# Kernel optimization log

Measured on AMD Instinct MI355X. Metric: run time of the kernel, lower is better.

The kernel has to match this reference:

```python
import jax, jax.numpy as jnp
import numpy as np

N_NODES = 100000
N_EDGES = 1600000
NIN = 128
NOUT = 128


def setup_inputs() -> dict:
    key = jax.random.key(0)
    k1, k2, k3, k4, k5 = jax.random.split(key, 5)
    x = jax.random.normal(k1, (N_NODES, NIN), dtype=jnp.float32)
    edge_index = jax.random.randint(k2, (2, N_EDGES), 0, N_NODES, dtype=jnp.int32)
    edge_attr = jax.random.uniform(k3, (N_EDGES,), dtype=jnp.float32)
    # GCNConv linear weight (glorot-ish scale) and bias
    W = jax.random.normal(k4, (NIN, NOUT), dtype=jnp.float32) / np.sqrt(NIN)
    b = jnp.zeros((NOUT,), dtype=jnp.float32)
    return {"x": x, "edge_index": edge_index, "edge_attr": edge_attr, "W": W, "b": b}


def reference(x, edge_index, edge_attr, W, b):
    # PyG GCNConv: out = D^{-1/2} (A + I) D^{-1/2} X W + b
    # edge_attr is accepted by the wrapper's forward but ignored.
    N = x.shape[0]
    src, dst = edge_index[0], edge_index[1]
    # add self-loops
    loops = jnp.arange(N, dtype=edge_index.dtype)
    src = jnp.concatenate([src, loops])
    dst = jnp.concatenate([dst, loops])
    # degree over destination nodes (unit edge weights + self loops)
    deg = jax.ops.segment_sum(jnp.ones_like(dst, dtype=x.dtype), dst, num_segments=N)
    dinv = jnp.where(deg > 0, jax.lax.rsqrt(deg), 0.0)
    norm = dinv[src] * dinv[dst]  # [E + N]
    h = x @ W  # [N, NOUT] — project before aggregation (PyG order)
    msgs = h[src] * norm[:, None]  # [E + N, NOUT] gathered messages
    out = jax.ops.segment_sum(msgs, dst, num_segments=N) + b
    return out
```

## Files before the change

kernel.cpp:

```cpp
#include <hip/hip_runtime.h>
#include <hip/hip_bf16.h>


#define NIN 128
#define NOUT 128
#define NPART 8
#define SCAT_B 256
#define MAXD 64

typedef __attribute__((ext_vector_type(8))) short short8;
typedef __attribute__((ext_vector_type(4))) float f32x4;

__device__ __forceinline__ float bf2f(unsigned short u) {
    unsigned v = ((unsigned)u) << 16;
    return __uint_as_float(v);
}
__device__ __forceinline__ unsigned short f2bf(float f) {
    unsigned u = __float_as_uint(f);
    unsigned r = 0x7FFFu + ((u >> 16) & 1u);
    return (unsigned short)((u + r) >> 16);
}

__global__ void k_scatter(const int* __restrict__ ei, int* __restrict__ cnt,
                          int* __restrict__ adj, int E, int N) {
    int p = blockIdx.x & (NPART - 1);
    int c = blockIdx.x / NPART;
    int PS = (N + NPART - 1) / NPART;
    int lo = p * PS, hi = min(N, lo + PS);
    int chunkE = (E + SCAT_B - 1) / SCAT_B;
    int e0 = c * chunkE, e1 = min(E, e0 + chunkE);
    for (int e = e0 + threadIdx.x; e < e1; e += 256) {
        int d = ei[E + e];
        if (d >= lo && d < hi) {
            int s = ei[e];
            int pos = atomicAdd(&cnt[d], 1);
            if (pos < MAXD) adj[(size_t)d * MAXD + pos] = s;
        }
    }
}

#define WT_PITCH 136
__global__ __launch_bounds__(256) void k_gemm(const float* __restrict__ x,
                                              const float* __restrict__ W,
                                              const int* __restrict__ cnt,
                                              unsigned short* __restrict__ h, int N) {
    __shared__ unsigned short Wt[128 * WT_PITCH];
    for (int idx = threadIdx.x; idx < NIN * NOUT; idx += 256) {
        int k = idx >> 7, n = idx & 127;
        Wt[n * WT_PITCH + k] = f2bf(W[idx]);
    }
    __syncthreads();

    int wave = threadIdx.x >> 6, lane = threadIdx.x & 63;
    int node_base = blockIdx.x * 64 + wave * 16;
    if (node_base >= N) return;

    int c = lane & 15, quad = lane >> 4;

    short8 a[4];
    const float4* xrow = (const float4*)(x + (size_t)(node_base + c) * NIN + quad * 8);
    #pragma unroll
    for (int kt = 0; kt < 4; kt++) {
        float4 f0 = xrow[kt * 8];
        float4 f1 = xrow[kt * 8 + 1];
        short8 af;
        af[0] = (short)f2bf(f0.x); af[1] = (short)f2bf(f0.y);
        af[2] = (short)f2bf(f0.z); af[3] = (short)f2bf(f0.w);
        af[4] = (short)f2bf(f1.x); af[5] = (short)f2bf(f1.y);
        af[6] = (short)f2bf(f1.z); af[7] = (short)f2bf(f1.w);
        a[kt] = af;
    }

    f32x4 acc[8];
    #pragma unroll
    for (int nt = 0; nt < 8; nt++) acc[nt] = (f32x4)(0.0f);

    #pragma unroll
    for (int nt = 0; nt < 8; nt++) {
        const unsigned short* wp = &Wt[(nt * 16 + c) * WT_PITCH + quad * 8];
        #pragma unroll
        for (int kt = 0; kt < 4; kt++) {
            short8 bfrag = *(const short8*)(wp + kt * 32);
            acc[nt] = __builtin_amdgcn_mfma_f32_16x16x32_bf16(a[kt], bfrag, acc[nt], 0, 0, 0);
        }
    }

    float dv[4];
    #pragma unroll
    for (int r = 0; r < 4; r++)
        dv[r] = rsqrtf((float)(cnt[node_base + quad * 4 + r] + 1));

    #pragma unroll
    for (int nt = 0; nt < 8; nt++) {
        #pragma unroll
        for (int r = 0; r < 4; r++) {
            int node = node_base + quad * 4 + r;
            h[(size_t)node * NOUT + nt * 16 + c] = f2bf(acc[nt][r] * dv[r]);
        }
    }
}

__global__ __launch_bounds__(256) void k_agg(const unsigned short* __restrict__ h,
                                             const int* __restrict__ cnt,
                                             const int* __restrict__ adj,
                                             const float* __restrict__ bias,
                                             float* __restrict__ out, int N) {
    int wave = threadIdx.x >> 6, lane = threadIdx.x & 63;
    int half = lane >> 5, sub = lane & 31;
    int node = blockIdx.x * 4 + wave;
    if (node >= N) return;

    int degree = cnt[node];
    float dn = rsqrtf((float)(degree + 1));
    int e0 = node * MAXD;
    int e1 = e0 + min(degree, MAXD);

    const uint2* hp = (const uint2*)h;
    float a0 = 0.f, a1 = 0.f, a2 = 0.f, a3 = 0.f;

    {
        int s = half ? ((e0 < e1) ? adj[e0] : node) : node;
        uint2 v = hp[(size_t)s * 32 + sub];
        if (!half || (e0 < e1)) {
            a0 += bf2f((unsigned short)(v.x & 0xFFFF));
            a1 += bf2f((unsigned short)(v.x >> 16));
            a2 += bf2f((unsigned short)(v.y & 0xFFFF));
            a3 += bf2f((unsigned short)(v.y >> 16));
        }
    }

    int e = e0 + 1;
    for (; e + 7 < e1; e += 8) {
        #pragma unroll
        for (int k = 0; k < 4; k++) {
            int s = adj[e + 2 * k + half];
            uint2 v = hp[(size_t)s * 32 + sub];
            a0 += bf2f((unsigned short)(v.x & 0xFFFF));
            a1 += bf2f((unsigned short)(v.x >> 16));
            a2 += bf2f((unsigned short)(v.y & 0xFFFF));
            a3 += bf2f((unsigned short)(v.y >> 16));
        }
    }
    for (; e + 1 < e1; e += 2) {
        int s = adj[e + half];
        uint2 v = hp[(size_t)s * 32 + sub];
        a0 += bf2f((unsigned short)(v.x & 0xFFFF));
        a1 += bf2f((unsigned short)(v.x >> 16));
        a2 += bf2f((unsigned short)(v.y & 0xFFFF));
        a3 += bf2f((unsigned short)(v.y >> 16));
    }
    if (e < e1) {
        int s = adj[e];
        uint2 v = hp[(size_t)s * 32 + sub];
        if (!half) {
            a0 += bf2f((unsigned short)(v.x & 0xFFFF));
            a1 += bf2f((unsigned short)(v.x >> 16));
            a2 += bf2f((unsigned short)(v.y & 0xFFFF));
            a3 += bf2f((unsigned short)(v.y >> 16));
        }
    }

    a0 += __shfl_xor(a0, 32);
    a1 += __shfl_xor(a1, 32);
    a2 += __shfl_xor(a2, 32);
    a3 += __shfl_xor(a3, 32);

    if (!half) {
        float4 b4 = ((const float4*)bias)[sub];
        f32x4 o;
        o[0] = a0 * dn + b4.x;
        o[1] = a1 * dn + b4.y;
        o[2] = a2 * dn + b4.z;
        o[3] = a3 * dn + b4.w;
        __builtin_nontemporal_store(o, (f32x4*)(out + (size_t)node * NOUT) + sub);
    }
}

static inline size_t align256(size_t v) { return (v + 255) & ~(size_t)255; }

extern "C" void kernel_launch(void* const* d_in, const int* in_sizes, int n_in,
                              void* d_out, int out_size, void* d_ws, size_t ws_size,
                              hipStream_t stream) {
    const float* x  = (const float*)d_in[0];
    const int*   ei = (const int*)d_in[1];
    const float* W  = (const float*)d_in[3];
    const float* b  = (const float*)d_in[4];
    float*       out = (float*)d_out;

    int N = in_sizes[0] / NIN;
    int E = in_sizes[1] / 2;

    char* ws = (char*)d_ws;
    size_t o = 0;
    int*   cnt = (int*)(ws + o);   o += align256((size_t)N * 4);
    int*   adj = (int*)(ws + o);   o += align256((size_t)N * MAXD * 4);
    unsigned short* h = (unsigned short*)(ws + o); o += align256((size_t)N * NOUT * 2);
    (void)ws_size; (void)n_in; (void)out_size;

    hipMemsetAsync(cnt, 0, (size_t)N * 4, stream);
    k_scatter<<<NPART * SCAT_B, 256, 0, stream>>>(ei, cnt, adj, E, N);
    k_gemm<<<(N + 63) / 64, 256, 0, stream>>>(x, W, cnt, h, N);
    k_agg<<<(N + 3) / 4, 256, 0, stream>>>(h, cnt, adj, b, out, N);
}
```

Measured before the change: 277.2 us.

## Fuse edge scatter and GEMM into one kernel, move source normalization to aggregation

Merges the adjacency-building scatter and the X·W projection into a single launch, interleaving scatter and GEMM blocks so both run concurrently. Because the GEMM can no longer wait for the degree counts, it stores unnormalized h, and the aggregation kernel now looks up cnt[s] and computes rsqrt per gathered neighbor. The scatter also reads edges with vectorized nontemporal 4-wide loads, and x is loaded nontemporally. This removes a kernel boundary and overlaps the two phases, at the cost of an extra random cnt gather plus an rsqrt per edge in the aggregation.

```diff
diff --git a/kernel.cpp b/kernel.cpp
--- a/kernel.cpp
+++ b/kernel.cpp
@@ -7,9 +7,12 @@
 #define NPART 8
 #define SCAT_B 256
 #define MAXD 64
+#define WT_PITCH 136
 
 typedef __attribute__((ext_vector_type(8))) short short8;
 typedef __attribute__((ext_vector_type(4))) float f32x4;
+typedef __attribute__((ext_vector_type(4))) int   i32x4;
+typedef __attribute__((ext_vector_type(4))) float f32x4v;
 
 __device__ __forceinline__ float bf2f(unsigned short u) {
     unsigned v = ((unsigned)u) << 16;
@@ -21,30 +24,43 @@
     return (unsigned short)((u + r) >> 16);
 }
 
-__global__ void k_scatter(const int* __restrict__ ei, int* __restrict__ cnt,
-                          int* __restrict__ adj, int E, int N) {
-    int p = blockIdx.x & (NPART - 1);
-    int c = blockIdx.x / NPART;
-    int PS = (N + NPART - 1) / NPART;
-    int lo = p * PS, hi = min(N, lo + PS);
-    int chunkE = (E + SCAT_B - 1) / SCAT_B;
-    int e0 = c * chunkE, e1 = min(E, e0 + chunkE);
-    for (int e = e0 + threadIdx.x; e < e1; e += 256) {
-        int d = ei[E + e];
-        if (d >= lo && d < hi) {
-            int s = ei[e];
-            int pos = atomicAdd(&cnt[d], 1);
-            if (pos < MAXD) adj[(size_t)d * MAXD + pos] = s;
-        }
-    }
-}
-
-#define WT_PITCH 136
-__global__ __launch_bounds__(256) void k_gemm(const float* __restrict__ x,
-                                              const float* __restrict__ W,
-                                              const int* __restrict__ cnt,
-                                              unsigned short* __restrict__ h, int N) {
+__global__ __launch_bounds__(256) void k_build(const float* __restrict__ x,
+                                               const float* __restrict__ W,
+                                               const int* __restrict__ ei,
+                                               int* __restrict__ cnt,
+                                               int* __restrict__ adj,
+                                               unsigned short* __restrict__ h,
+                                               int E, int N, int gb) {
     __shared__ unsigned short Wt[128 * WT_PITCH];
+
+    int grp   = blockIdx.x >> 4;
+    int lane8 = blockIdx.x & 7;
+    int rid   = grp * 8 + lane8;
+
+    if ((blockIdx.x >> 3) & 1) {
+        int p = lane8;
+        int c = grp;
+        int PS = (N + NPART - 1) / NPART;
+        int lo = p * PS, hi = min(N, lo + PS);
+        int chunkE = (((E + SCAT_B - 1) / SCAT_B) + 3) & ~3;
+        int e0 = c * chunkE, e1 = min(E, e0 + chunkE);
+        for (int e = e0 + (int)threadIdx.x * 4; e < e1; e += 1024) {
+            i32x4 s4 = __builtin_nontemporal_load((const i32x4*)(ei + e));
+            i32x4 d4 = __builtin_nontemporal_load((const i32x4*)(ei + E + e));
+            #pragma unroll
+            for (int k = 0; k < 4; k++) {
+                int d = d4[k];
+                if (d >= lo && d < hi) {
+                    int pos = atomicAdd(&cnt[d], 1);
+                    if (pos < MAXD) adj[(size_t)d * MAXD + pos] = s4[k];
+                }
+            }
+        }
+        return;
+    }
+
+    if (rid >= gb) return;
+
     for (int idx = threadIdx.x; idx < NIN * NOUT; idx += 256) {
         int k = idx >> 7, n = idx & 127;
         Wt[n * WT_PITCH + k] = f2bf(W[idx]);
@@ -52,22 +68,22 @@
     __syncthreads();
 
     int wave = threadIdx.x >> 6, lane = threadIdx.x & 63;
-    int node_base = blockIdx.x * 64 + wave * 16;
+    int node_base = rid * 64 + wave * 16;
     if (node_base >= N) return;
 
     int c = lane & 15, quad = lane >> 4;
 
     short8 a[4];
-    const float4* xrow = (const float4*)(x + (size_t)(node_base + c) * NIN + quad * 8);
+    const f32x4v* xrow = (const f32x4v*)(x + (size_t)(node_base + c) * NIN + quad * 8);
     #pragma unroll
     for (int kt = 0; kt < 4; kt++) {
-        float4 f0 = xrow[kt * 8];
-        float4 f1 = xrow[kt * 8 + 1];
+        f32x4v f0 = __builtin_nontemporal_load(xrow + kt * 8);
+        f32x4v f1 = __builtin_nontemporal_load(xrow + kt * 8 + 1);
         short8 af;
-        af[0] = (short)f2bf(f0.x); af[1] = (short)f2bf(f0.y);
-        af[2] = (short)f2bf(f0.z); af[3] = (short)f2bf(f0.w);
-        af[4] = (short)f2bf(f1.x); af[5] = (short)f2bf(f1.y);
-        af[6] = (short)f2bf(f1.z); af[7] = (short)f2bf(f1.w);
+        af[0] = (short)f2bf(f0[0]); af[1] = (short)f2bf(f0[1]);
+        af[2] = (short)f2bf(f0[2]); af[3] = (short)f2bf(f0[3]);
+        af[4] = (short)f2bf(f1[0]); af[5] = (short)f2bf(f1[1]);
+        af[6] = (short)f2bf(f1[2]); af[7] = (short)f2bf(f1[3]);
         a[kt] = af;
     }
 
@@ -85,17 +101,12 @@
         }
     }
 
-    float dv[4];
-    #pragma unroll
-    for (int r = 0; r < 4; r++)
-        dv[r] = rsqrtf((float)(cnt[node_base + quad * 4 + r] + 1));
-
     #pragma unroll
     for (int nt = 0; nt < 8; nt++) {
         #pragma unroll
         for (int r = 0; r < 4; r++) {
             int node = node_base + quad * 4 + r;
-            h[(size_t)node * NOUT + nt * 16 + c] = f2bf(acc[nt][r] * dv[r]);
+            h[(size_t)node * NOUT + nt * 16 + c] = f2bf(acc[nt][r]);
         }
     }
 }
@@ -110,23 +121,25 @@
     int node = blockIdx.x * 4 + wave;
     if (node >= N) return;
 
-    int degree = cnt[node];
-    float dn = rsqrtf((float)(degree + 1));
+    int degc = cnt[node];
+    float dn = rsqrtf((float)(degc + 1));
     int e0 = node * MAXD;
-    int e1 = e0 + min(degree, MAXD);
+    int e1 = e0 + min(degc, MAXD);
 
     const uint2* hp = (const uint2*)h;
     float a0 = 0.f, a1 = 0.f, a2 = 0.f, a3 = 0.f;
 
     {
-        int s = half ? ((e0 < e1) ? adj[e0] : node) : node;
+        int s = node; float ds = dn;
+        if (half) {
+            if (e0 < e1) { s = adj[e0]; ds = rsqrtf((float)(cnt[s] + 1)); }
+            else ds = 0.f;
+        }
         uint2 v = hp[(size_t)s * 32 + sub];
-        if (!half || (e0 < e1)) {
-            a0 += bf2f((unsigned short)(v.x & 0xFFFF));
-            a1 += bf2f((unsigned short)(v.x >> 16));
-            a2 += bf2f((unsigned short)(v.y & 0xFFFF));
-            a3 += bf2f((unsigned short)(v.y >> 16));
-        }
+        a0 += bf2f((unsigned short)(v.x & 0xFFFF)) * ds;
+        a1 += bf2f((unsigned short)(v.x >> 16)) * ds;
+        a2 += bf2f((unsigned short)(v.y & 0xFFFF)) * ds;
+        a3 += bf2f((unsigned short)(v.y >> 16)) * ds;
     }
 
     int e = e0 + 1;
@@ -134,29 +147,32 @@
         #pragma unroll
         for (int k = 0; k < 4; k++) {
             int s = adj[e + 2 * k + half];
+            float ds = rsqrtf((float)(cnt[s] + 1));
             uint2 v = hp[(size_t)s * 32 + sub];
-            a0 += bf2f((unsigned short)(v.x & 0xFFFF));
-            a1 += bf2f((unsigned short)(v.x >> 16));
-            a2 += bf2f((unsigned short)(v.y & 0xFFFF));
-            a3 += bf2f((unsigned short)(v.y >> 16));
+            a0 += bf2f((unsigned short)(v.x & 0xFFFF)) * ds;
+            a1 += bf2f((unsigned short)(v.x >> 16)) * ds;
+            a2 += bf2f((unsigned short)(v.y & 0xFFFF)) * ds;
+            a3 += bf2f((unsigned short)(v.y >> 16)) * ds;
         }
     }
     for (; e + 1 < e1; e += 2) {
         int s = adj[e + half];
+        float ds = rsqrtf((float)(cnt[s] + 1));
         uint2 v = hp[(size_t)s * 32 + sub];
-        a0 += bf2f((unsigned short)(v.x & 0xFFFF));
-        a1 += bf2f((unsigned short)(v.x >> 16));
-        a2 += bf2f((unsigned short)(v.y & 0xFFFF));
-        a3 += bf2f((unsigned short)(v.y >> 16));
+        a0 += bf2f((unsigned short)(v.x & 0xFFFF)) * ds;
+        a1 += bf2f((unsigned short)(v.x >> 16)) * ds;
+        a2 += bf2f((unsigned short)(v.y & 0xFFFF)) * ds;
+        a3 += bf2f((unsigned short)(v.y >> 16)) * ds;
     }
     if (e < e1) {
         int s = adj[e];
         uint2 v = hp[(size_t)s * 32 + sub];
         if (!half) {
-            a0 += bf2f((unsigned short)(v.x & 0xFFFF));
-            a1 += bf2f((unsigned short)(v.x >> 16));
-            a2 += bf2f((unsigned short)(v.y & 0xFFFF));
-            a3 += bf2f((unsigned short)(v.y >> 16));
+            float ds = rsqrtf((float)(cnt[s] + 1));
+            a0 += bf2f((unsigned short)(v.x & 0xFFFF)) * ds;
+            a1 += bf2f((unsigned short)(v.x >> 16)) * ds;
+            a2 += bf2f((unsigned short)(v.y & 0xFFFF)) * ds;
+            a3 += bf2f((unsigned short)(v.y >> 16)) * ds;
         }
     }
 
@@ -189,6 +205,7 @@
 
     int N = in_sizes[0] / NIN;
     int E = in_sizes[1] / 2;
+    int gb = (N + 63) / 64;
 
     char* ws = (char*)d_ws;
     size_t o = 0;
@@ -198,7 +215,6 @@
     (void)ws_size; (void)n_in; (void)out_size;
 
     hipMemsetAsync(cnt, 0, (size_t)N * 4, stream);
-    k_scatter<<<NPART * SCAT_B, 256, 0, stream>>>(ei, cnt, adj, E, N);
-    k_gemm<<<(N + 63) / 64, 256, 0, stream>>>(x, W, cnt, h, N);
+    k_build<<<16 * SCAT_B, 256, 0, stream>>>(x, W, ei, cnt, adj, h, E, N, gb);
     k_agg<<<(N + 3) / 4, 256, 0, stream>>>(h, cnt, adj, b, out, N);
 }
```

After: 300.3 us. 1.08x slower.
